# Kernel optimization log

Measured on AMD Instinct MI355X. Metric: run time of the kernel, lower is better.

The kernel has to match this reference:

```python
import jax, jax.numpy as jnp
import numpy as np

# dims: B=batch, N1=in_channels (primary caps), P=pcap_n_dims, N2=n_caps, D=n_dims
B, N1, P, N2, D = 64, 1152, 8, 128, 16
ROUTINGS = 2


def squash(s, axis=-1):
    # squash_factor * unit_vector, with eps-stabilized norm (matches torch.finfo eps)
    sq_norm = jnp.sum(s * s, axis=axis, keepdims=True)
    norm = jnp.sqrt(sq_norm + jnp.finfo(s.dtype).eps)
    return (sq_norm / (1.0 + sq_norm)) * (s / norm)


def setup_inputs() -> dict:
    key = jax.random.key(0)
    k1, k2 = jax.random.split(key)
    x = jax.random.normal(k1, (B, N1, P), dtype=jnp.float32)
    # learned transform W: nn.Parameter(torch.randn(1, N1, N2, D, P)); leading 1 dropped
    W = jax.random.normal(k2, (N1, N2, D, P), dtype=jnp.float32)
    return {"x": x, "W": W}


def reference(x, W):
    b, n1 = x.shape[0], x.shape[1]
    n2 = W.shape[1]
    # caps2_predicted[b,i,n,d] = sum_p W[i,n,d,p] * x[b,i,p]  (the tiled batched matmul)
    pred = jnp.einsum('indp,bip->bind', W, x)  # [B, N1, N2, D]
    raw = jnp.zeros((b, n1, n2), dtype=pred.dtype)  # routing logits
    v = None
    for i in range(ROUTINGS):
        c = jax.nn.softmax(raw, axis=2)                  # softmax over output capsules
        s = jnp.einsum('bin,bind->bnd', c, pred)         # weighted sum over input caps
        v = squash(s, axis=-1)                           # [B, N2, D]
        if i < ROUTINGS - 1:
            # agreement: <prediction, output> over the D dimension
            raw = raw + jnp.einsum('bind,bnd->bin', pred, v)
    return v  # [B, n_caps, n_dims]
```

## Files before the change

kernel.cpp:

```cpp
#include <hip/hip_runtime.h>
#include <math.h>

#define B_   64
#define N1_  1152
#define P_   8
#define N2_  128
#define D_   16

#define NSPLIT 32
#define CHUNK  (N1_ / NSPLIT)
#define NIB    (CHUNK / 4)

typedef __attribute__((ext_vector_type(8)))  short bf16x8;
typedef __attribute__((ext_vector_type(4)))  float f32x4;
typedef __attribute__((ext_vector_type(16))) float f32x16;

__device__ inline void split_frag(float4 a0, float4 a1, bf16x8& hi, bf16x8& lo)
{
    float w[8] = {a0.x, a0.y, a0.z, a0.w, a1.x, a1.y, a1.z, a1.w};
#pragma unroll
    for (int j = 0; j < 8; ++j) {
        unsigned ub = __float_as_uint(w[j]);
        hi[j] = (short)(ub >> 16);
        float hif = __uint_as_float(ub & 0xffff0000u);
        float r = w[j] - hif;
        lo[j] = (short)(__float_as_uint(r) >> 16);
    }
}

__device__ inline void split_arr(const float* w, bf16x8& hi, bf16x8& lo)
{
#pragma unroll
    for (int j = 0; j < 8; ++j) {
        unsigned ub = __float_as_uint(w[j]);
        hi[j] = (short)(ub >> 16);
        float hif = __uint_as_float(ub & 0xffff0000u);
        float r = w[j] - hif;
        lo[j] = (short)(__float_as_uint(r) >> 16);
    }
}

__global__ __launch_bounds__(128) void k0_xt(const float* __restrict__ x,
                                             float* __restrict__ xt)
{
    const int i  = blockIdx.x;
    const int t  = threadIdx.x;
    const int b  = t >> 1, ph = t & 1;
    float4 v = *(const float4*)(x + ((size_t)b * N1_ + i) * P_ + ph * 4);
    *(float4*)(xt + ((size_t)i * 64 + b) * P_ + ph * 4) = v;
}

__global__ __launch_bounds__(256) void k1_s0_mfma(const float* __restrict__ xt,
                                                  const float* __restrict__ W,
                                                  float* __restrict__ s0p)
{
    const int tid   = threadIdx.x;
    const int lane  = tid & 63;
    const int wv    = tid >> 6;
    const int col   = lane & 15;
    const int quad  = lane >> 4;
    const int b     = wv * 16 + col;
    const int nbase = blockIdx.x * 4;
    const int isp   = blockIdx.y;
    const int ibase = isp * CHUNK;

    f32x4 acc[4];
#pragma unroll
    for (int nn = 0; nn < 4; ++nn) acc[nn] = (f32x4){0.f, 0.f, 0.f, 0.f};

    const float* xlane = xt + (size_t)(ibase + quad) * (64 * P_) + b * P_;

    for (int ib = 0; ib < NIB; ++ib) {
        const int i0 = ibase + ib * 4;
        float4 xa = *(const float4*)(xlane);
        float4 xb = *(const float4*)(xlane + 4);
        xlane += 4 * 64 * P_;
        bf16x8 bhi, blo;
        split_frag(xa, xb, bhi, blo);
#pragma unroll
        for (int nn = 0; nn < 4; ++nn) {
            const float* wp = W + (((size_t)(i0 + quad) * N2_ + nbase + nn) * D_ + col) * P_;
            float4 wa = *(const float4*)wp;
            float4 wb = *(const float4*)(wp + 4);
            bf16x8 ahi, alo;
            split_frag(wa, wb, ahi, alo);
            acc[nn] = __builtin_amdgcn_mfma_f32_16x16x32_bf16(ahi, bhi, acc[nn], 0, 0, 0);
            acc[nn] = __builtin_amdgcn_mfma_f32_16x16x32_bf16(ahi, blo, acc[nn], 0, 0, 0);
            acc[nn] = __builtin_amdgcn_mfma_f32_16x16x32_bf16(alo, bhi, acc[nn], 0, 0, 0);
        }
    }
#pragma unroll
    for (int nn = 0; nn < 4; ++nn) {
        float4 v = make_float4(acc[nn][0], acc[nn][1], acc[nn][2], acc[nn][3]);
        *(float4*)(s0p + (size_t)isp * (B_ * N2_ * D_) + (size_t)b * (N2_ * D_)
                   + (nbase + nn) * D_ + quad * 4) = v;
    }
}

__global__ __launch_bounds__(256) void k2_squash(const float* __restrict__ spart,
                                                 float* __restrict__ vout,
                                                 float scale, int nsplit)
{
    int idx = blockIdx.x * 256 + threadIdx.x;
    float s = 0.f;
    for (int sp = 0; sp < nsplit; ++sp)
        s += spart[(size_t)sp * (B_ * N2_ * D_) + idx];
    s *= scale;
    float sq = s * s;
    sq += __shfl_xor(sq, 1);
    sq += __shfl_xor(sq, 2);
    sq += __shfl_xor(sq, 4);
    sq += __shfl_xor(sq, 8);
    float norm = sqrtf(sq + 1.1920929e-7f);
    vout[idx] = (sq / (1.f + sq)) * (s / norm);
}

__global__ __launch_bounds__(256, 4) void k3a_mfma32(const float* __restrict__ xt,
                                                     const float* __restrict__ W,
                                                     const float* __restrict__ v0,
                                                     float* __restrict__ raw_t)
{
    const int tid  = threadIdx.x;
    const int lane = tid & 63;
    const int wv   = tid >> 6;
    const int m    = lane & 31;
    const int kh   = lane >> 5;
    const int isub = m >> 3;
    const int p    = m & 7;
    const int n    = blockIdx.x;
    const int ichunk = blockIdx.y * 64;
    const int src  = 2 * m + kh;

    bf16x8 vhi[2], vlo[2];
#pragma unroll
    for (int bt = 0; bt < 2; ++bt) {
        const float* vp = v0 + (size_t)(bt * 32 + m) * (N2_ * D_) + n * D_ + kh * 8;
        float4 qa = *(const float4*)vp;
        float4 qb = *(const float4*)(vp + 4);
        split_frag(qa, qb, vhi[bt], vlo[bt]);
    }

#pragma unroll
    for (int k4 = 0; k4 < 4; ++k4) {
        const int i0 = ichunk + (wv + 4 * k4) * 4;
        const float* wp = W + ((size_t)(i0 + isub) * N2_ + n) * (D_ * P_) + kh * 64 + p;
        float a[8];
#pragma unroll
        for (int j = 0; j < 8; ++j) a[j] = wp[8 * j];
        bf16x8 ahi, alo;
        split_arr(a, ahi, alo);

        f32x16 acc0, acc1;
#pragma unroll
        for (int r = 0; r < 16; ++r) { acc0[r] = 0.f; acc1[r] = 0.f; }
        acc0 = __builtin_amdgcn_mfma_f32_32x32x16_bf16(ahi, vhi[0], acc0, 0, 0, 0);
        acc0 = __builtin_amdgcn_mfma_f32_32x32x16_bf16(ahi, vlo[0], acc0, 0, 0, 0);
        acc0 = __builtin_amdgcn_mfma_f32_32x32x16_bf16(alo, vhi[0], acc0, 0, 0, 0);
        acc1 = __builtin_amdgcn_mfma_f32_32x32x16_bf16(ahi, vhi[1], acc1, 0, 0, 0);
        acc1 = __builtin_amdgcn_mfma_f32_32x32x16_bf16(ahi, vlo[1], acc1, 0, 0, 0);
        acc1 = __builtin_amdgcn_mfma_f32_32x32x16_bf16(alo, vhi[1], acc1, 0, 0, 0);

#pragma unroll
        for (int is = 0; is < 4; ++is) {
            const float4* xrow = (const float4*)(xt + (size_t)(i0 + is) * (64 * P_));
            float4 xl0 = xrow[lane];
            float4 xl1 = xrow[64 + lane];
            float4 xs0, xs1;
            xs0.x = __shfl(xl0.x, src); xs0.y = __shfl(xl0.y, src);
            xs0.z = __shfl(xl0.z, src); xs0.w = __shfl(xl0.w, src);
            xs1.x = __shfl(xl1.x, src); xs1.y = __shfl(xl1.y, src);
            xs1.z = __shfl(xl1.z, src); xs1.w = __shfl(xl1.w, src);

            float r0 = acc0[4 * is] * xs0.x + acc0[4 * is + 1] * xs0.y
                     + acc0[4 * is + 2] * xs0.z + acc0[4 * is + 3] * xs0.w;
            float r1 = acc1[4 * is] * xs1.x + acc1[4 * is + 1] * xs1.y
                     + acc1[4 * is + 2] * xs1.z + acc1[4 * is + 3] * xs1.w;
            r0 += __shfl_xor(r0, 32);
            r1 += __shfl_xor(r1, 32);
            if (kh == 0) {
                raw_t[(size_t)(i0 + is) * (N2_ * 64) + n * 64 + m]      = r0;
                raw_t[(size_t)(i0 + is) * (N2_ * 64) + n * 64 + 32 + m] = r1;
            }
        }
    }
}

__global__ __launch_bounds__(256) void k3b_t(float* __restrict__ rawc)
{
    const int i  = blockIdx.x;
    const int t  = threadIdx.x;
    const int b  = t & 63;
    const int ng = t >> 6;
    float* base = rawc + (size_t)i * (N2_ * 64) + b;

    float v[32];
    float m = -1e30f;
#pragma unroll
    for (int k = 0; k < 32; ++k) {
        v[k] = base[(ng * 32 + k) * 64];
        m = fmaxf(m, v[k]);
    }
    __shared__ float red[4][64];
    red[ng][b] = m;
    __syncthreads();
    m = fmaxf(fmaxf(red[0][b], red[1][b]), fmaxf(red[2][b], red[3][b]));
    float s = 0.f;
#pragma unroll
    for (int k = 0; k < 32; ++k) { v[k] = __expf(v[k] - m); s += v[k]; }
    __syncthreads();
    red[ng][b] = s;
    __syncthreads();
    s = red[0][b] + red[1][b] + red[2][b] + red[3][b];
    float inv = 1.f / s;
#pragma unroll
    for (int k = 0; k < 32; ++k)
        base[(ng * 32 + k) * 64] = v[k] * inv;
}

__global__ __launch_bounds__(256) void k3c_s1_mfma(const float* __restrict__ xt,
                                                   const float* __restrict__ W,
                                                   const float* __restrict__ c_t,
                                                   float* __restrict__ s1p)
{
    const int tid   = threadIdx.x;
    const int lane  = tid & 63;
    const int wv    = tid >> 6;
    const int col   = lane & 15;
    const int quad  = lane >> 4;
    const int n     = blockIdx.x * 4 + wv;
    const int isp   = blockIdx.y;
    const int ibase = isp * CHUNK;

    f32x4 acc[4];
#pragma unroll
    for (int bt = 0; bt < 4; ++bt) acc[bt] = (f32x4){0.f, 0.f, 0.f, 0.f};

    for (int ib = 0; ib < NIB; ++ib) {
        const int iq = ibase + ib * 4 + quad;
        const float* wp = W + ((size_t)iq * N2_ + n) * (D_ * P_) + col * P_;
        float4 wa = *(const float4*)wp;
        float4 wb = *(const float4*)(wp + 4);
        bf16x8 ahi, alo;
        split_frag(wa, wb, ahi, alo);
#pragma unroll
        for (int bt = 0; bt < 4; ++bt) {
            const int b = bt * 16 + col;
            const float* xp = xt + (size_t)iq * (64 * P_) + b * P_;
            float4 xa = *(const float4*)xp;
            float4 xb = *(const float4*)(xp + 4);
            float c = c_t[((size_t)iq * N2_ + n) * 64 + b];
            float4 ya = make_float4(xa.x * c, xa.y * c, xa.z * c, xa.w * c);
            float4 yb = make_float4(xb.x * c, xb.y * c, xb.z * c, xb.w * c);
            bf16x8 bhi, blo;
            split_frag(ya, yb, bhi, blo);
            acc[bt] = __builtin_amdgcn_mfma_f32_16x16x32_bf16(ahi, bhi, acc[bt], 0, 0, 0);
            acc[bt] = __builtin_amdgcn_mfma_f32_16x16x32_bf16(ahi, blo, acc[bt], 0, 0, 0);
            acc[bt] = __builtin_amdgcn_mfma_f32_16x16x32_bf16(alo, bhi, acc[bt], 0, 0, 0);
        }
    }
#pragma unroll
    for (int bt = 0; bt < 4; ++bt) {
        const int b = bt * 16 + col;
        float4 v = make_float4(acc[bt][0], acc[bt][1], acc[bt][2], acc[bt][3]);
        *(float4*)(s1p + (size_t)isp * (B_ * N2_ * D_) + (size_t)b * (N2_ * D_)
                   + n * D_ + quad * 4) = v;
    }
}

extern "C" void kernel_launch(void* const* d_in, const int* in_sizes, int n_in,
                              void* d_out, int out_size, void* d_ws, size_t ws_size,
                              hipStream_t stream)
{
    const float* x = (const float*)d_in[0];
    const float* W = (const float*)d_in[1];
    float* out = (float*)d_out;

    float* s_part = (float*)d_ws;
    float* v0     = s_part + (size_t)NSPLIT * B_ * N2_ * D_;
    float* c_t    = v0 + B_ * N2_ * D_;
    float* xt     = c_t + (size_t)N1_ * N2_ * 64;

    k0_xt       <<<N1_,              128, 0, stream>>>(x, xt);
    k1_s0_mfma  <<<dim3(32, NSPLIT), 256, 0, stream>>>(xt, W, s_part);
    k2_squash   <<<512,              256, 0, stream>>>(s_part, v0, 1.f / 128.f, NSPLIT);
    k3a_mfma32  <<<dim3(128, 18),    256, 0, stream>>>(xt, W, v0, c_t);
    k3b_t       <<<N1_,              256, 0, stream>>>(c_t);
    k3c_s1_mfma <<<dim3(32, NSPLIT), 256, 0, stream>>>(xt, W, c_t, s_part);
    k2_squash   <<<512,              256, 0, stream>>>(s_part, out, 1.f, NSPLIT);
}
```

Baseline: 205.4 us.

## Fuse agreement logits with exp and atomic softmax denominators, drop softmax kernel

The separate softmax kernel goes away. The agreement kernel now writes exp(logit) directly and accumulates per-(i,b) denominators with atomics into a buffer zeroed in the transpose kernel. The routing-weighted sum kernel divides by that denominator on the fly. Without max subtraction the exp could overflow for large logits, though at this problem's scales the values are probably bounded. It also halves NSPLIT, vectorises the squash kernel to float4, and retiles the agreement kernel over n with x held in registers.

```diff
diff --git a/kernel.cpp b/kernel.cpp
--- a/kernel.cpp
+++ b/kernel.cpp
@@ -7,7 +7,7 @@
 #define N2_  128
 #define D_   16
 
-#define NSPLIT 32
+#define NSPLIT 16
 #define CHUNK  (N1_ / NSPLIT)
 #define NIB    (CHUNK / 4)
 
@@ -41,13 +41,16 @@
 }
 
 __global__ __launch_bounds__(128) void k0_xt(const float* __restrict__ x,
-                                             float* __restrict__ xt)
+                                             float* __restrict__ xt,
+                                             float* __restrict__ denom)
 {
     const int i  = blockIdx.x;
     const int t  = threadIdx.x;
     const int b  = t >> 1, ph = t & 1;
     float4 v = *(const float4*)(x + ((size_t)b * N1_ + i) * P_ + ph * 4);
     *(float4*)(xt + ((size_t)i * 64 + b) * P_ + ph * 4) = v;
+    int z = i * 128 + t;
+    if (z < N1_ * 64) denom[z] = 0.f;
 }
 
 __global__ __launch_bounds__(256) void k1_s0_mfma(const float* __restrict__ xt,
@@ -102,23 +105,26 @@
                                                  float scale, int nsplit)
 {
     int idx = blockIdx.x * 256 + threadIdx.x;
-    float s = 0.f;
-    for (int sp = 0; sp < nsplit; ++sp)
-        s += spart[(size_t)sp * (B_ * N2_ * D_) + idx];
-    s *= scale;
-    float sq = s * s;
+    float4 s = make_float4(0.f, 0.f, 0.f, 0.f);
+    for (int sp = 0; sp < nsplit; ++sp) {
+        float4 t = *(const float4*)(spart + (size_t)sp * (B_ * N2_ * D_) + (size_t)idx * 4);
+        s.x += t.x; s.y += t.y; s.z += t.z; s.w += t.w;
+    }
+    s.x *= scale; s.y *= scale; s.z *= scale; s.w *= scale;
+    float sq = s.x * s.x + s.y * s.y + s.z * s.z + s.w * s.w;
     sq += __shfl_xor(sq, 1);
     sq += __shfl_xor(sq, 2);
-    sq += __shfl_xor(sq, 4);
-    sq += __shfl_xor(sq, 8);
     float norm = sqrtf(sq + 1.1920929e-7f);
-    vout[idx] = (sq / (1.f + sq)) * (s / norm);
-}
-
-__global__ __launch_bounds__(256, 4) void k3a_mfma32(const float* __restrict__ xt,
-                                                     const float* __restrict__ W,
-                                                     const float* __restrict__ v0,
-                                                     float* __restrict__ raw_t)
+    float f = (sq / (1.f + sq)) / norm;
+    float4 o = make_float4(s.x * f, s.y * f, s.z * f, s.w * f);
+    *(float4*)(vout + (size_t)idx * 4) = o;
+}
+
+__global__ __launch_bounds__(256) void k3a2_mfma32(const float* __restrict__ xt,
+                                                   const float* __restrict__ W,
+                                                   const float* __restrict__ v0,
+                                                   float* __restrict__ e_t,
+                                                   float* __restrict__ denom)
 {
     const int tid  = threadIdx.x;
     const int lane = tid & 63;
@@ -127,22 +133,32 @@
     const int kh   = lane >> 5;
     const int isub = m >> 3;
     const int p    = m & 7;
-    const int n    = blockIdx.x;
-    const int ichunk = blockIdx.y * 64;
-    const int src  = 2 * m + kh;
-
-    bf16x8 vhi[2], vlo[2];
-#pragma unroll
-    for (int bt = 0; bt < 2; ++bt) {
-        const float* vp = v0 + (size_t)(bt * 32 + m) * (N2_ * D_) + n * D_ + kh * 8;
-        float4 qa = *(const float4*)vp;
-        float4 qb = *(const float4*)(vp + 4);
-        split_frag(qa, qb, vhi[bt], vlo[bt]);
-    }
-
-#pragma unroll
-    for (int k4 = 0; k4 < 4; ++k4) {
-        const int i0 = ichunk + (wv + 4 * k4) * 4;
+    const int i0   = blockIdx.y * 4;
+    const int nbase = blockIdx.x * 32 + wv * 8;
+
+    float4 xq0[4], xq1[4];
+#pragma unroll
+    for (int is = 0; is < 4; ++is) {
+        const float* xp = xt + (size_t)(i0 + is) * (64 * P_) + m * 8 + kh * 4;
+        xq0[is] = *(const float4*)xp;
+        xq1[is] = *(const float4*)(xp + 256);
+    }
+
+    float dacc[4] = {0.f, 0.f, 0.f, 0.f};
+
+#pragma unroll 1
+    for (int nt = 0; nt < 8; ++nt) {
+        const int n = nbase + nt;
+
+        bf16x8 vhi[2], vlo[2];
+#pragma unroll
+        for (int bt = 0; bt < 2; ++bt) {
+            const float* vp = v0 + (size_t)(bt * 32 + m) * (N2_ * D_) + n * D_ + kh * 8;
+            float4 qa = *(const float4*)vp;
+            float4 qb = *(const float4*)(vp + 4);
+            split_frag(qa, qb, vhi[bt], vlo[bt]);
+        }
+
         const float* wp = W + ((size_t)(i0 + isub) * N2_ + n) * (D_ * P_) + kh * 64 + p;
         float a[8];
 #pragma unroll
@@ -162,64 +178,34 @@
 
 #pragma unroll
         for (int is = 0; is < 4; ++is) {
-            const float4* xrow = (const float4*)(xt + (size_t)(i0 + is) * (64 * P_));
-            float4 xl0 = xrow[lane];
-            float4 xl1 = xrow[64 + lane];
-            float4 xs0, xs1;
-            xs0.x = __shfl(xl0.x, src); xs0.y = __shfl(xl0.y, src);
-            xs0.z = __shfl(xl0.z, src); xs0.w = __shfl(xl0.w, src);
-            xs1.x = __shfl(xl1.x, src); xs1.y = __shfl(xl1.y, src);
-            xs1.z = __shfl(xl1.z, src); xs1.w = __shfl(xl1.w, src);
-
-            float r0 = acc0[4 * is] * xs0.x + acc0[4 * is + 1] * xs0.y
-                     + acc0[4 * is + 2] * xs0.z + acc0[4 * is + 3] * xs0.w;
-            float r1 = acc1[4 * is] * xs1.x + acc1[4 * is + 1] * xs1.y
-                     + acc1[4 * is + 2] * xs1.z + acc1[4 * is + 3] * xs1.w;
+            float r0 = acc0[4 * is] * xq0[is].x + acc0[4 * is + 1] * xq0[is].y
+                     + acc0[4 * is + 2] * xq0[is].z + acc0[4 * is + 3] * xq0[is].w;
+            float r1 = acc1[4 * is] * xq1[is].x + acc1[4 * is + 1] * xq1[is].y
+                     + acc1[4 * is + 2] * xq1[is].z + acc1[4 * is + 3] * xq1[is].w;
             r0 += __shfl_xor(r0, 32);
             r1 += __shfl_xor(r1, 32);
-            if (kh == 0) {
-                raw_t[(size_t)(i0 + is) * (N2_ * 64) + n * 64 + m]      = r0;
-                raw_t[(size_t)(i0 + is) * (N2_ * 64) + n * 64 + 32 + m] = r1;
-            }
-        }
-    }
-}
-
-__global__ __launch_bounds__(256) void k3b_t(float* __restrict__ rawc)
-{
-    const int i  = blockIdx.x;
-    const int t  = threadIdx.x;
-    const int b  = t & 63;
-    const int ng = t >> 6;
-    float* base = rawc + (size_t)i * (N2_ * 64) + b;
-
-    float v[32];
-    float m = -1e30f;
-#pragma unroll
-    for (int k = 0; k < 32; ++k) {
-        v[k] = base[(ng * 32 + k) * 64];
-        m = fmaxf(m, v[k]);
-    }
-    __shared__ float red[4][64];
-    red[ng][b] = m;
+            float e = __expf(kh ? r1 : r0);
+            e_t[(size_t)(i0 + is) * (N2_ * 64) + n * 64 + kh * 32 + m] = e;
+            dacc[is] += e;
+        }
+    }
+
+    __shared__ float dred[4][4][64];
+#pragma unroll
+    for (int is = 0; is < 4; ++is) dred[wv][is][kh * 32 + m] = dacc[is];
     __syncthreads();
-    m = fmaxf(fmaxf(red[0][b], red[1][b]), fmaxf(red[2][b], red[3][b]));
-    float s = 0.f;
-#pragma unroll
-    for (int k = 0; k < 32; ++k) { v[k] = __expf(v[k] - m); s += v[k]; }
-    __syncthreads();
-    red[ng][b] = s;
-    __syncthreads();
-    s = red[0][b] + red[1][b] + red[2][b] + red[3][b];
-    float inv = 1.f / s;
-#pragma unroll
-    for (int k = 0; k < 32; ++k)
-        base[(ng * 32 + k) * 64] = v[k] * inv;
+    {
+        const int is = tid >> 6;
+        const int b  = tid & 63;
+        float s = dred[0][is][b] + dred[1][is][b] + dred[2][is][b] + dred[3][is][b];
+        atomicAdd(&denom[(size_t)(i0 + is) * 64 + b], s);
+    }
 }
 
 __global__ __launch_bounds__(256) void k3c_s1_mfma(const float* __restrict__ xt,
                                                    const float* __restrict__ W,
-                                                   const float* __restrict__ c_t,
+                                                   const float* __restrict__ e_t,
+                                                   const float* __restrict__ denom,
                                                    float* __restrict__ s1p)
 {
     const int tid   = threadIdx.x;
@@ -248,7 +234,9 @@
             const float* xp = xt + (size_t)iq * (64 * P_) + b * P_;
             float4 xa = *(const float4*)xp;
             float4 xb = *(const float4*)(xp + 4);
-            float c = c_t[((size_t)iq * N2_ + n) * 64 + b];
+            float e  = e_t[((size_t)iq * N2_ + n) * 64 + b];
+            float dv = denom[(size_t)iq * 64 + b];
+            float c  = e * __builtin_amdgcn_rcpf(dv);
             float4 ya = make_float4(xa.x * c, xa.y * c, xa.z * c, xa.w * c);
             float4 yb = make_float4(xb.x * c, xb.y * c, xb.z * c, xb.w * c);
             bf16x8 bhi, blo;
@@ -277,14 +265,14 @@
 
     float* s_part = (float*)d_ws;
     float* v0     = s_part + (size_t)NSPLIT * B_ * N2_ * D_;
-    float* c_t    = v0 + B_ * N2_ * D_;
-    float* xt     = c_t + (size_t)N1_ * N2_ * 64;
-
-    k0_xt       <<<N1_,              128, 0, stream>>>(x, xt);
-    k1_s0_mfma  <<<dim3(32, NSPLIT), 256, 0, stream>>>(xt, W, s_part);
-    k2_squash   <<<512,              256, 0, stream>>>(s_part, v0, 1.f / 128.f, NSPLIT);
-    k3a_mfma32  <<<dim3(128, 18),    256, 0, stream>>>(xt, W, v0, c_t);
-    k3b_t       <<<N1_,              256, 0, stream>>>(c_t);
-    k3c_s1_mfma <<<dim3(32, NSPLIT), 256, 0, stream>>>(xt, W, c_t, s_part);
-    k2_squash   <<<512,              256, 0, stream>>>(s_part, out, 1.f, NSPLIT);
-}
+    float* e_t    = v0 + B_ * N2_ * D_;
+    float* xt     = e_t + (size_t)N1_ * N2_ * 64;
+    float* denom  = xt + (size_t)N1_ * 64 * P_;
+
+    k0_xt       <<<N1_,               128, 0, stream>>>(x, xt, denom);
+    k1_s0_mfma  <<<dim3(32, NSPLIT),  256, 0, stream>>>(xt, W, s_part);
+    k2_squash   <<<128,               256, 0, stream>>>(s_part, v0, 1.f / 128.f, NSPLIT);
+    k3a2_mfma32 <<<dim3(4, N1_ / 4),  256, 0, stream>>>(xt, W, v0, e_t, denom);
+    k3c_s1_mfma <<<dim3(32, NSPLIT),  256, 0, stream>>>(xt, W, e_t, denom, s_part);
+    k2_squash   <<<128,               256, 0, stream>>>(s_part, out, 1.f, NSPLIT);
+}
```

Result: faster. 185.9 us (-9.5%).
